# Kernel optimization log

Hardware: AMD Instinct MI355X
Metric: run time of the kernel (lower is better)

## Reference

```python
import jax, jax.numpy as jnp
import numpy as np

N = 50000
IN_F = 128
OUT_F = 128
NRELA = 128
E1 = 400000
E2 = 100000
ALPHA = 0.2   # LeakyReLU slope
D = 0.85      # PageRank damping
EPS = 1e-12


def setup_inputs() -> dict:
    key = jax.random.key(0)
    ks = jax.random.split(key, 8)
    return {
        "input": jax.random.normal(ks[0], (N, IN_F), dtype=jnp.float32),
        "edge": jax.random.randint(ks[1], (2, E1), 0, N, dtype=jnp.int64),
        "edge_embed": jax.random.normal(ks[2], (E1, NRELA), dtype=jnp.float32),
        "edge_list_nhop": jax.random.randint(ks[3], (2, E2), 0, N, dtype=jnp.int64),
        "edge_embed_nhop": jax.random.normal(ks[4], (E2, NRELA), dtype=jnp.float32),
        "entity_rank": jax.random.uniform(ks[5], (N,), dtype=jnp.float32),
        "a": 0.05 * jax.random.normal(ks[6], (OUT_F, 2 * IN_F + NRELA), dtype=jnp.float32),
        "a_2": 0.05 * jax.random.normal(ks[7], (1, OUT_F), dtype=jnp.float32),
    }


def reference(input, edge, edge_embed, edge_list_nhop, edge_embed_nhop, entity_rank, a, a_2):
    n = input.shape[0]
    # concat n-hop edges (len(edge_list_nhop) != 0 path in the original)
    e = jnp.concatenate([edge, edge_list_nhop], axis=1)          # [2, E]
    emb = jnp.concatenate([edge_embed, edge_embed_nhop], axis=0) # [E, nrela]
    src, dst = e[0], e[1]

    # edge MLP: edge_h = [x_src | x_dst | rel]  -> a @ edge_h^T, leakyrelu
    edge_h = jnp.concatenate([input[src], input[dst], emb], axis=1)   # [E, 2*in+nrela]
    edge_m = jax.nn.leaky_relu(edge_h @ a.T, ALPHA)                   # [E, out]
    powers = -jax.nn.leaky_relu(edge_m @ a_2[0], ALPHA)               # [E]
    edge_e = jnp.exp(powers)                                          # [E]

    # softmax-like normalization over incoming edges of each target node
    a_rowsum = jax.ops.segment_sum(edge_e, dst, num_segments=n)       # [N]
    a_rowsum = jnp.where(a_rowsum == 0.0, EPS, a_rowsum)
    rel_att = edge_e / a_rowsum[dst]                                  # [E]

    # PageRank-style rank update
    e_rowsum = jax.ops.segment_sum(rel_att, src, num_segments=n)      # [N] (out-sum)
    e_rowsum = jnp.where(e_rowsum == 0.0, EPS, e_rowsum)
    val = rel_att * entity_rank[src] / e_rowsum[src]                  # [E]
    e_colsum = jax.ops.segment_sum(val, dst, num_segments=n)          # [N]
    new_rank = 1.0 - D + D * e_colsum                                 # [N]

    # rank-weighted attention propagation of edge features
    edge_prop = (rel_att * new_rank[src])[:, None] * edge_m           # [E, out]
    h_prime = jax.ops.segment_sum(edge_prop, dst, num_segments=n)     # [N, out]

    return jax.nn.elu(h_prime), new_rank
```

## Files before the change

### kernel.cpp

```cpp
#include <hip/hip_runtime.h>
#include <math.h>

#define N_NODES 50000
#define E1N 400000
#define E2N 100000
#define E_TOT 500000
#define ALPHAC 0.2f
#define DAMP 0.85f
#define EPSC 1e-12f

typedef __bf16 bf16_t;
typedef __bf16 bf16x4 __attribute__((ext_vector_type(4)));
typedef __bf16 bf16x8 __attribute__((ext_vector_type(8)));
typedef float f32x16 __attribute__((ext_vector_type(16)));

__device__ __forceinline__ float lrelu(float x) { return x > 0.f ? x : ALPHAC * x; }

__global__ __launch_bounds__(256) void k_pack12(const float* __restrict__ a,
                                                bf16_t* __restrict__ bp) {
  int i = blockIdx.x * 256 + threadIdx.x;
  if (i >= 32768) return;
  int j = i & 7;
  int l = (i >> 3) & 63;
  int nt = (i >> 9) & 7;
  int ks = i >> 12;
  int c = nt * 32 + (l & 31);
  int o = (c < 128) ? c : c - 128;
  int koff = (c < 128) ? 0 : 128;
  int k = ks * 16 + ((l >> 5) << 3) + j;
  bp[i] = (bf16_t)a[o * 384 + koff + k];
}

__global__ __launch_bounds__(256) void k_pack3(const float* __restrict__ a,
                                               bf16_t* __restrict__ bp) {
  int i = blockIdx.x * 256 + threadIdx.x;
  if (i >= 16384) return;
  int j = i & 7;
  int l = (i >> 3) & 63;
  int nt = (i >> 9) & 3;
  int ks = i >> 11;
  int o = nt * 32 + (l & 31);
  int k = ks * 16 + ((l >> 5) << 3) + j;
  bp[i] = (bf16_t)a[o * 384 + 256 + k];
}

__global__ __launch_bounds__(256) void k_edges(const int* __restrict__ edge,
                                               const int* __restrict__ nhop,
                                               int* __restrict__ sidx,
                                               int* __restrict__ didx, int stride,
                                               int* __restrict__ cnt) {
  int e = blockIdx.x * 256 + threadIdx.x;
  if (e >= E_TOT) return;
  int s, d;
  if (e < E1N) {
    s = edge[(size_t)e * stride];
    d = edge[(size_t)(E1N + e) * stride];
  } else {
    int t = e - E1N;
    s = nhop[(size_t)t * stride];
    d = nhop[(size_t)(E2N + t) * stride];
  }
  sidx[e] = s;
  didx[e] = d;
  if (cnt) atomicAdd(&cnt[d], 1);
}

__global__ __launch_bounds__(256) void k_scan(const int* __restrict__ cnt,
                                              int* __restrict__ csr_start,
                                              int* __restrict__ cursor) {
  __shared__ int ls[256];
  __shared__ int lofs[256];
  int t = threadIdx.x;
  int lo = t * 196, hi = lo + 196;
  if (hi > N_NODES) hi = N_NODES;
  int s = 0;
  for (int i = lo; i < hi; ++i) s += cnt[i];
  ls[t] = s;
  __syncthreads();
  if (t == 0) {
    int run = 0;
    for (int i = 0; i < 256; ++i) { lofs[i] = run; run += ls[i]; }
  }
  __syncthreads();
  int run = lofs[t];
  for (int i = lo; i < hi; ++i) {
    csr_start[i] = run;
    cursor[i] = run;
    run += cnt[i];
  }
}

__global__ __launch_bounds__(256) void k_pos(const int* __restrict__ didx,
                                             int* __restrict__ cursor,
                                             int* __restrict__ eid) {
  int e = blockIdx.x * 256 + threadIdx.x;
  if (e >= E_TOT) return;
  int pos = atomicAdd(&cursor[didx[e]], 1);
  eid[pos] = e;
}

__global__ __launch_bounds__(256) void k_uv(const float* __restrict__ input,
                                            const bf16_t* __restrict__ bp12,
                                            bf16_t* __restrict__ uv) {
  const int tid = threadIdx.x, lane = tid & 63, wv = tid >> 6;
  const int n0 = blockIdx.x * 128 + wv * 32;
  const int m = lane & 31, hi2 = lane >> 5;
  int n = n0 + m;
  if (n >= N_NODES) n = 0;
  const float* ar = input + (size_t)n * 128 + hi2 * 8;
  const bf16x8* bp = (const bf16x8*)bp12;

  f32x16 acc[8];
#pragma unroll
  for (int nt = 0; nt < 8; ++nt)
#pragma unroll
    for (int r = 0; r < 16; ++r) acc[nt][r] = 0.f;

#pragma unroll
  for (int ks = 0; ks < 8; ++ks) {
    float4 u0 = *(const float4*)(ar + ks * 16);
    float4 u1 = *(const float4*)(ar + ks * 16 + 4);
    bf16x8 af = {(bf16_t)u0.x, (bf16_t)u0.y, (bf16_t)u0.z, (bf16_t)u0.w,
                 (bf16_t)u1.x, (bf16_t)u1.y, (bf16_t)u1.z, (bf16_t)u1.w};
#pragma unroll
    for (int nt = 0; nt < 8; ++nt)
      acc[nt] = __builtin_amdgcn_mfma_f32_32x32x16_bf16(af, bp[(ks * 8 + nt) * 64 + lane],
                                                        acc[nt], 0, 0, 0);
  }
#pragma unroll
  for (int nt = 0; nt < 8; ++nt)
#pragma unroll
    for (int r = 0; r < 16; ++r) {
      int row = (r & 3) + ((r >> 2) << 3) + (hi2 << 2);
      int node = n0 + row;
      if (node < N_NODES) uv[(size_t)node * 256 + nt * 32 + m] = (bf16_t)acc[nt][r];
    }
}

__global__ __launch_bounds__(256, 3) void k_passA(
    const float* __restrict__ eemb, const float* __restrict__ eembn,
    const bf16_t* __restrict__ uv, const int* __restrict__ sidx,
    const int* __restrict__ didx, const bf16_t* __restrict__ bp3,
    const float* __restrict__ a2, float* __restrict__ edge_e,
    float* __restrict__ a_rowsum, bf16_t* __restrict__ P) {
  __shared__ bf16_t s_sum[128][136];
  const int tid = threadIdx.x;
  const long long e0 = (long long)blockIdx.x * 128;

  {
    const int g = tid >> 5;
    const int cl = (tid & 31) * 4;
#pragma unroll
    for (int i = 0; i < 16; ++i) {
      int el = i * 8 + g;
      long long e = e0 + el;
      float sx = 0.f, sy = 0.f, sz = 0.f, sw = 0.f;
      if (e < E_TOT) {
        int s = sidx[e], d = didx[e];
        bf16x4 u = *(const bf16x4*)(uv + (size_t)s * 256 + cl);
        bf16x4 v = *(const bf16x4*)(uv + (size_t)d * 256 + 128 + cl);
        sx = (float)u[0] + (float)v[0];
        sy = (float)u[1] + (float)v[1];
        sz = (float)u[2] + (float)v[2];
        sw = (float)u[3] + (float)v[3];
      }
      bf16x4 o = {(bf16_t)sx, (bf16_t)sy, (bf16_t)sz, (bf16_t)sw};
      *(bf16x4*)&s_sum[el][cl] = o;
    }
  }
  __syncthreads();

  const int lane = tid & 63;
  const int wv = tid >> 6;
  const long long e0w = e0 + wv * 32;
  if (e0w >= E_TOT) return;
  const int m = lane & 31, hi2 = lane >> 5;
  const long long e = e0w + m;
  const float* b2 = (e < E1N) ? (eemb + (size_t)e * 128)
                              : (eembn + (size_t)(e - E1N) * 128);
  const float* ar = b2 + hi2 * 8;

  const bf16x8* bp = (const bf16x8*)bp3;
  f32x16 acc[4];
#pragma unroll
  for (int nt = 0; nt < 4; ++nt)
#pragma unroll
    for (int r = 0; r < 16; ++r) acc[nt][r] = 0.f;

  auto loadA = [&](int ks) -> bf16x8 {
    float4 u0 = *(const float4*)(ar + ks * 16);
    float4 u1 = *(const float4*)(ar + ks * 16 + 4);
    bf16x8 rr = {(bf16_t)u0.x, (bf16_t)u0.y, (bf16_t)u0.z, (bf16_t)u0.w,
                 (bf16_t)u1.x, (bf16_t)u1.y, (bf16_t)u1.z, (bf16_t)u1.w};
    return rr;
  };

  bf16x8 a_cur = loadA(0);
  bf16x8 bb[4], bn[4];
#pragma unroll
  for (int nt = 0; nt < 4; ++nt) bb[nt] = bp[nt * 64 + lane];

#pragma unroll
  for (int ks = 0; ks < 8; ++ks) {
    bf16x8 a_nxt;
    if (ks < 7) {
      a_nxt = loadA(ks + 1);
#pragma unroll
      for (int nt = 0; nt < 4; ++nt) bn[nt] = bp[((ks + 1) * 4 + nt) * 64 + lane];
    }
#pragma unroll
    for (int nt = 0; nt < 4; ++nt)
      acc[nt] = __builtin_amdgcn_mfma_f32_32x32x16_bf16(a_cur, bb[nt], acc[nt], 0, 0, 0);
    a_cur = a_nxt;
#pragma unroll
    for (int nt = 0; nt < 4; ++nt) bb[nt] = bn[nt];
  }

  bf16_t* Pt = P + ((long long)blockIdx.x * 4 + wv) * 4096;
  float sac[16];
#pragma unroll
  for (int r = 0; r < 16; ++r) sac[r] = 0.f;
#pragma unroll
  for (int nt = 0; nt < 4; ++nt) {
    int o = nt * 32 + m;
    float a2v = a2[o];
#pragma unroll
    for (int r = 0; r < 16; ++r) {
      int row = (r & 3) + ((r >> 2) << 3) + (hi2 << 2);
      float c = acc[nt][r] + (float)s_sum[wv * 32 + row][o];
      float p = lrelu(c);
      Pt[(nt * 16 + r) * 64 + lane] = (bf16_t)p;
      sac[r] += p * a2v;
    }
  }
#pragma unroll
  for (int off = 1; off < 32; off <<= 1) {
#pragma unroll
    for (int r = 0; r < 16; ++r) sac[r] += __shfl_xor(sac[r], off, 64);
  }
  if (m == 0) {
#pragma unroll
    for (int r = 0; r < 16; ++r) {
      int row = (r & 3) + ((r >> 2) << 3) + (hi2 << 2);
      long long ee_i = e0w + row;
      float ev = expf(-lrelu(sac[r]));
      edge_e[ee_i] = ev;
      atomicAdd(&a_rowsum[didx[ee_i]], ev);
    }
  }
}

__global__ __launch_bounds__(256) void k_hprime(const bf16_t* __restrict__ P,
                                                const int* __restrict__ eid,
                                                const int* __restrict__ csr_start,
                                                const int* __restrict__ cnt,
                                                const float* __restrict__ w,
                                                float* __restrict__ out) {
  int g = (blockIdx.x << 3) | (threadIdx.x >> 5);
  if (g >= N_NODES) return;
  int m = threadIdx.x & 31;
  int start = csr_start[g], deg = cnt[g];
  float a0 = 0.f, a1 = 0.f, a2v = 0.f, a3v = 0.f;
  for (int i = 0; i < deg; ++i) {
    int e = eid[start + i];
    float we = w[e];
    int row = e & 31;
    int r = (row & 3) | ((row >> 3) << 2);
    int hi2 = (row >> 2) & 1;
    const bf16_t* p = P + (long long)(e >> 5) * 4096 + r * 64 + hi2 * 32 + m;
    a0 += we * (float)p[0];
    a1 += we * (float)p[16 * 64];
    a2v += we * (float)p[32 * 64];
    a3v += we * (float)p[48 * 64];
  }
  float* o = out + (size_t)g * 128 + m;
  o[0] = a0 > 0.f ? a0 : expm1f(a0);
  o[32] = a1 > 0.f ? a1 : expm1f(a1);
  o[64] = a2v > 0.f ? a2v : expm1f(a2v);
  o[96] = a3v > 0.f ? a3v : expm1f(a3v);
}

template <bool ACCUM>
__global__ __launch_bounds__(256, 3) void k_pass(
    const float* __restrict__ eemb, const float* __restrict__ eembn,
    const bf16_t* __restrict__ uv, const int* __restrict__ sidx,
    const int* __restrict__ didx, const bf16_t* __restrict__ bp3,
    const float* __restrict__ a2, float* __restrict__ edge_e,
    float* __restrict__ a_rowsum, const float* __restrict__ rel_att,
    const float* __restrict__ new_rank, float* __restrict__ hout) {
  __shared__ bf16_t s_sum[128][136];
  const int tid = threadIdx.x;
  const long long e0 = (long long)blockIdx.x * 128;
  {
    const int g = tid >> 5;
    const int cl = (tid & 31) * 4;
#pragma unroll
    for (int i = 0; i < 16; ++i) {
      int el = i * 8 + g;
      long long e = e0 + el;
      float sx = 0.f, sy = 0.f, sz = 0.f, sw = 0.f;
      if (e < E_TOT) {
        int s = sidx[e], d = didx[e];
        bf16x4 u = *(const bf16x4*)(uv + (size_t)s * 256 + cl);
        bf16x4 v = *(const bf16x4*)(uv + (size_t)d * 256 + 128 + cl);
        sx = (float)u[0] + (float)v[0];
        sy = (float)u[1] + (float)v[1];
        sz = (float)u[2] + (float)v[2];
        sw = (float)u[3] + (float)v[3];
      }
      bf16x4 o = {(bf16_t)sx, (bf16_t)sy, (bf16_t)sz, (bf16_t)sw};
      *(bf16x4*)&s_sum[el][cl] = o;
    }
  }
  __syncthreads();

  const int lane = tid & 63;
  const int wv = tid >> 6;
  const long long e0w = e0 + wv * 32;
  if (e0w >= E_TOT) return;
  const int m = lane & 31, hi2 = lane >> 5;
  const long long e = e0w + m;
  const float* b2 = (e < E1N) ? (eemb + (size_t)e * 128)
                              : (eembn + (size_t)(e - E1N) * 128);
  const float* ar = b2 + hi2 * 8;

  const bf16x8* bp = (const bf16x8*)bp3;
  f32x16 acc[4];
#pragma unroll
  for (int nt = 0; nt < 4; ++nt)
#pragma unroll
    for (int r = 0; r < 16; ++r) acc[nt][r] = 0.f;

  auto loadA = [&](int ks) -> bf16x8 {
    float4 u0 = *(const float4*)(ar + ks * 16);
    float4 u1 = *(const float4*)(ar + ks * 16 + 4);
    bf16x8 rr = {(bf16_t)u0.x, (bf16_t)u0.y, (bf16_t)u0.z, (bf16_t)u0.w,
                 (bf16_t)u1.x, (bf16_t)u1.y, (bf16_t)u1.z, (bf16_t)u1.w};
    return rr;
  };

  bf16x8 a_cur = loadA(0);
  bf16x8 bb[4], bn[4];
#pragma unroll
  for (int nt = 0; nt < 4; ++nt) bb[nt] = bp[nt * 64 + lane];

#pragma unroll
  for (int ks = 0; ks < 8; ++ks) {
    bf16x8 a_nxt;
    if (ks < 7) {
      a_nxt = loadA(ks + 1);
#pragma unroll
      for (int nt = 0; nt < 4; ++nt) bn[nt] = bp[((ks + 1) * 4 + nt) * 64 + lane];
    }
#pragma unroll
    for (int nt = 0; nt < 4; ++nt)
      acc[nt] = __builtin_amdgcn_mfma_f32_32x32x16_bf16(a_cur, bb[nt], acc[nt], 0, 0, 0);
    a_cur = a_nxt;
#pragma unroll
    for (int nt = 0; nt < 4; ++nt) bb[nt] = bn[nt];
  }

  if (!ACCUM) {
    float sac[16];
#pragma unroll
    for (int r = 0; r < 16; ++r) sac[r] = 0.f;
#pragma unroll
    for (int nt = 0; nt < 4; ++nt) {
      float a2v = a2[nt * 32 + m];
      int o = nt * 32 + m;
#pragma unroll
      for (int r = 0; r < 16; ++r) {
        int row = (r & 3) + ((r >> 2) << 3) + (hi2 << 2);
        float c = acc[nt][r] + (float)s_sum[wv * 32 + row][o];
        sac[r] += lrelu(c) * a2v;
      }
    }
#pragma unroll
    for (int off = 1; off < 32; off <<= 1) {
#pragma unroll
      for (int r = 0; r < 16; ++r) sac[r] += __shfl_xor(sac[r], off, 64);
    }
    if (m == 0) {
#pragma unroll
      for (int r = 0; r < 16; ++r) {
        int row = (r & 3) + ((r >> 2) << 3) + (hi2 << 2);
        long long ee_i = e0w + row;
        float ev = expf(-lrelu(sac[r]));
        edge_e[ee_i] = ev;
        atomicAdd(&a_rowsum[didx[ee_i]], ev);
      }
    }
  } else {
    float w_m = rel_att[e] * new_rank[sidx[e]];
    int d = didx[e];
    float wr[16];
    int dr[16];
#pragma unroll
    for (int r = 0; r < 16; ++r) {
      int row = (r & 3) + ((r >> 2) << 3) + (hi2 << 2);
      wr[r] = __shfl(w_m, row, 64);
      dr[r] = __shfl(d, row, 64);
    }
#pragma unroll
    for (int nt = 0; nt < 4; ++nt) {
      int o = nt * 32 + m;
#pragma unroll
      for (int r = 0; r < 16; ++r) {
        int row = (r & 3) + ((r >> 2) << 3) + (hi2 << 2);
        float c = acc[nt][r] + (float)s_sum[wv * 32 + row][o];
        atomicAdd(&hout[(size_t)dr[r] * 128 + o], lrelu(c) * wr[r]);
      }
    }
  }
}

__global__ __launch_bounds__(256) void k_relatt(const float* __restrict__ edge_e,
                                                const int* __restrict__ didx,
                                                const int* __restrict__ sidx,
                                                const float* __restrict__ a_rowsum,
                                                float* __restrict__ rel_att,
                                                float* __restrict__ e_rowsum) {
  int e = blockIdx.x * 256 + threadIdx.x;
  if (e >= E_TOT) return;
  float rs = a_rowsum[didx[e]];
  rs = (rs == 0.f) ? EPSC : rs;
  float r = edge_e[e] / rs;
  rel_att[e] = r;
  atomicAdd(&e_rowsum[sidx[e]], r);
}

__global__ __launch_bounds__(256) void k_val(const float* __restrict__ rel_att,
                                             const int* __restrict__ sidx,
                                             const int* __restrict__ didx,
                                             const float* __restrict__ rank,
                                             const float* __restrict__ e_rowsum,
                                             float* __restrict__ e_colsum) {
  int e = blockIdx.x * 256 + threadIdx.x;
  if (e >= E_TOT) return;
  int s = sidx[e];
  float er = e_rowsum[s];
  er = (er == 0.f) ? EPSC : er;
  float val = rel_att[e] * rank[s] / er;
  atomicAdd(&e_colsum[didx[e]], val);
}

__global__ __launch_bounds__(256) void k_rank(const float* __restrict__ e_colsum,
                                              float* __restrict__ new_rank,
                                              float* __restrict__ out_tail) {
  int n = blockIdx.x * 256 + threadIdx.x;
  if (n >= N_NODES) return;
  float nr = 1.f - DAMP + DAMP * e_colsum[n];
  new_rank[n] = nr;
  out_tail[n] = nr;
}

__global__ __launch_bounds__(256) void k_w(const float* __restrict__ rel_att,
                                           const int* __restrict__ sidx,
                                           const float* __restrict__ new_rank,
                                           float* __restrict__ w) {
  int e = blockIdx.x * 256 + threadIdx.x;
  if (e < E_TOT) w[e] = rel_att[e] * new_rank[sidx[e]];
}

__global__ __launch_bounds__(256) void k_elu(float* __restrict__ h) {
  int i = blockIdx.x * 256 + threadIdx.x;
  if (i < N_NODES * 128) {
    float x = h[i];
    h[i] = x > 0.f ? x : expm1f(x);
  }
}

extern "C" void kernel_launch(void* const* d_in, const int* in_sizes, int n_in,
                              void* d_out, int out_size, void* d_ws, size_t ws_size,
                              hipStream_t stream) {
  const float* input = (const float*)d_in[0];
  const int* edge = (const int*)d_in[1];
  const float* eemb = (const float*)d_in[2];
  const int* enh = (const int*)d_in[3];
  const float* eembn = (const float*)d_in[4];
  const float* rank = (const float*)d_in[5];
  const float* a = (const float*)d_in[6];
  const float* a2 = (const float*)d_in[7];
  float* out = (float*)d_out;

  int estride = (in_sizes[1] == 2 * E1N) ? 1 : 2;

  char* ws = (char*)d_ws;
  bf16_t* bp12 = (bf16_t*)(ws);
  bf16_t* bp3 = (bf16_t*)(ws + 65536);
  bf16_t* uv = (bf16_t*)(ws + 98304);
  int* sidx = (int*)(ws + 25698304);
  int* didx = (int*)(ws + 27698304);
  float* edge_e = (float*)(ws + 29698304);
  float* rel_att = (float*)(ws + 31698304);
  float* warr = (float*)(ws + 33698304);
  int* eid = (int*)(ws + 35698304);
  int* csr_start = (int*)(ws + 37698304);
  int* cursor = (int*)(ws + 37898304);
  int* cnt = (int*)(ws + 38098304);
  float* a_rowsum = (float*)(ws + 38298304);
  float* e_rowsum = (float*)(ws + 38498304);
  float* e_colsum = (float*)(ws + 38698304);
  float* new_rank = (float*)(ws + 38898304);
  bf16_t* P = (bf16_t*)(ws + 39098304);

  const bool big = ws_size >= 167098304ULL;

  const int NB = (E_TOT + 127) / 128;
  const int EB = (E_TOT + 255) / 256;

  if (big) {
    hipMemsetAsync(cnt, 0, 4 * 200000, stream);

    k_pack12<<<128, 256, 0, stream>>>(a, bp12);
    k_pack3<<<64, 256, 0, stream>>>(a, bp3);
    k_edges<<<EB, 256, 0, stream>>>(edge, enh, sidx, didx, estride, cnt);
    k_scan<<<1, 256, 0, stream>>>(cnt, csr_start, cursor);
    k_pos<<<EB, 256, 0, stream>>>(didx, cursor, eid);
    k_uv<<<(N_NODES + 127) / 128, 256, 0, stream>>>(input, bp12, uv);

    k_passA<<<NB, 256, 0, stream>>>(eemb, eembn, uv, sidx, didx, bp3, a2,
                                    edge_e, a_rowsum, P);
    k_relatt<<<EB, 256, 0, stream>>>(edge_e, didx, sidx, a_rowsum, rel_att, e_rowsum);
    k_val<<<EB, 256, 0, stream>>>(rel_att, sidx, didx, rank, e_rowsum, e_colsum);
    k_rank<<<(N_NODES + 255) / 256, 256, 0, stream>>>(e_colsum, new_rank,
                                                      out + (size_t)N_NODES * 128);
    k_w<<<EB, 256, 0, stream>>>(rel_att, sidx, new_rank, warr);
    k_hprime<<<(N_NODES + 7) / 8, 256, 0, stream>>>(P, eid, csr_start, cnt, warr, out);
  } else {
    hipMemsetAsync(cnt, 0, 4 * 200000, stream);
    hipMemsetAsync(out, 0, (size_t)N_NODES * 128 * 4, stream);

    k_pack12<<<128, 256, 0, stream>>>(a, bp12);
    k_pack3<<<64, 256, 0, stream>>>(a, bp3);
    k_edges<<<EB, 256, 0, stream>>>(edge, enh, sidx, didx, estride, nullptr);
    k_uv<<<(N_NODES + 127) / 128, 256, 0, stream>>>(input, bp12, uv);

    k_pass<false><<<NB, 256, 0, stream>>>(eemb, eembn, uv, sidx, didx, bp3, a2,
                                          edge_e, a_rowsum, nullptr, nullptr, nullptr);
    k_relatt<<<EB, 256, 0, stream>>>(edge_e, didx, sidx, a_rowsum, rel_att, e_rowsum);
    k_val<<<EB, 256, 0, stream>>>(rel_att, sidx, didx, rank, e_rowsum, e_colsum);
    k_rank<<<(N_NODES + 255) / 256, 256, 0, stream>>>(e_colsum, new_rank,
                                                      out + (size_t)N_NODES * 128);
    k_pass<true><<<NB, 256, 0, stream>>>(eemb, eembn, uv, sidx, didx, bp3, a2,
                                         nullptr, nullptr, rel_att, new_rank, out);
    k_elu<<<(N_NODES * 128 + 255) / 256, 256, 0, stream>>>(out);
  }
}
```

Before: 744.0 us.

## Split edge pass into coalesced relation GEMM and per-edge gather kernel

The fused per-edge pass is replaced by two kernels. The first computes the relation-embedding GEMM with A staged through swizzled shared memory and stores row-major fp16 results. The second gathers the node projections, applies LeakyReLU, writes bf16 activations in place, and computes edge_e with one atomic per edge. P now uses a row-major per-edge layout, so h_prime reads vectorised bf16x4 rows and computes the weight inline instead of calling a separate k_w kernel. The split adds an extra round trip of the 500k x 128 intermediate through global memory in exchange for coalesced accesses.

```diff
diff --git a/kernel.cpp b/kernel.cpp
--- a/kernel.cpp
+++ b/kernel.cpp
@@ -12,6 +12,9 @@
 typedef __bf16 bf16_t;
 typedef __bf16 bf16x4 __attribute__((ext_vector_type(4)));
 typedef __bf16 bf16x8 __attribute__((ext_vector_type(8)));
+typedef _Float16 f16_t;
+typedef _Float16 f16x4 __attribute__((ext_vector_type(4)));
+typedef _Float16 f16x8 __attribute__((ext_vector_type(8)));
 typedef float f32x16 __attribute__((ext_vector_type(16)));
 
 __device__ __forceinline__ float lrelu(float x) { return x > 0.f ? x : ALPHAC * x; }
@@ -137,16 +140,162 @@
     }
 }
 
-__global__ __launch_bounds__(256, 3) void k_passA(
+__global__ __launch_bounds__(256, 4) void k_gemm3(const float* __restrict__ eemb,
+                                                  const float* __restrict__ eembn,
+                                                  const bf16_t* __restrict__ bp3,
+                                                  f16_t* __restrict__ w3) {
+  __shared__ __align__(16) char s_raw[32768];
+  const int tid = threadIdx.x;
+  const long long e0 = (long long)blockIdx.x * 128;
+
+  {
+    const int r8 = tid >> 5;
+    const int cb = (tid & 31) * 8;
+#pragma unroll
+    for (int i = 0; i < 16; ++i) {
+      int row = i * 8 + r8;
+      long long e = e0 + row;
+      float4 u = {0.f, 0.f, 0.f, 0.f};
+      if (e < E_TOT) {
+        const float* src = (e < E1N) ? eemb + (size_t)e * 128
+                                     : eembn + (size_t)(e - E1N) * 128;
+        u = *(const float4*)(src + (cb >> 1));
+      }
+      bf16x4 b = {(bf16_t)u.x, (bf16_t)u.y, (bf16_t)u.z, (bf16_t)u.w};
+      *(bf16x4*)(s_raw + row * 256 + (cb ^ ((row & 7) << 4))) = b;
+    }
+  }
+  __syncthreads();
+
+  const int lane = tid & 63, wv = tid >> 6;
+  const int m = lane & 31, hi2 = lane >> 5;
+  const int arow = wv * 32 + m;
+  const int swz = (arow & 7) << 4;
+  const bf16x8* bp = (const bf16x8*)bp3;
+
+  f32x16 acc[4];
+#pragma unroll
+  for (int nt = 0; nt < 4; ++nt)
+#pragma unroll
+    for (int r = 0; r < 16; ++r) acc[nt][r] = 0.f;
+
+  bf16x8 bb[4], bn[4];
+#pragma unroll
+  for (int nt = 0; nt < 4; ++nt) bb[nt] = bp[nt * 64 + lane];
+
+#pragma unroll
+  for (int ks = 0; ks < 8; ++ks) {
+    bf16x8 af = *(const bf16x8*)(s_raw + arow * 256 + ((ks * 32 + hi2 * 16) ^ swz));
+    if (ks < 7) {
+#pragma unroll
+      for (int nt = 0; nt < 4; ++nt) bn[nt] = bp[((ks + 1) * 4 + nt) * 64 + lane];
+    }
+#pragma unroll
+    for (int nt = 0; nt < 4; ++nt)
+      acc[nt] = __builtin_amdgcn_mfma_f32_32x32x16_bf16(af, bb[nt], acc[nt], 0, 0, 0);
+#pragma unroll
+    for (int nt = 0; nt < 4; ++nt) bb[nt] = bn[nt];
+  }
+  __syncthreads();
+
+#pragma unroll
+  for (int nt = 0; nt < 4; ++nt)
+#pragma unroll
+    for (int r = 0; r < 16; ++r) {
+      int orow = (r & 3) + ((r >> 2) << 3) + (hi2 << 2);
+      int row = wv * 32 + orow;
+      int cb = (nt * 32 + m) * 2;
+      *(f16_t*)(s_raw + row * 256 + (cb ^ ((row & 7) << 4))) = (f16_t)acc[nt][r];
+    }
+  __syncthreads();
+
+  {
+    const int rr = tid >> 4;
+    const int cb = (tid & 15) * 16;
+#pragma unroll
+    for (int i = 0; i < 8; ++i) {
+      int row = i * 16 + rr;
+      long long e = e0 + row;
+      if (e < E_TOT) {
+        f16x8 v = *(const f16x8*)(s_raw + row * 256 + (cb ^ ((row & 7) << 4)));
+        *(f16x8*)(w3 + (size_t)e * 128 + (cb >> 1)) = v;
+      }
+    }
+  }
+}
+
+__global__ __launch_bounds__(256) void k_passB(const bf16_t* __restrict__ uv,
+                                               const int* __restrict__ sidx,
+                                               const int* __restrict__ didx,
+                                               f16_t* __restrict__ w3,
+                                               const float* __restrict__ a2,
+                                               float* __restrict__ edge_e,
+                                               float* __restrict__ a_rowsum) {
+  long long e = (long long)blockIdx.x * 8 + (threadIdx.x >> 5);
+  if (e >= E_TOT) return;
+  const int m = threadIdx.x & 31;
+  int s = sidx[e], d = didx[e];
+  bf16x4 u = *(const bf16x4*)(uv + (size_t)s * 256 + m * 4);
+  bf16x4 v = *(const bf16x4*)(uv + (size_t)d * 256 + 128 + m * 4);
+  f16x4 w = *(const f16x4*)(w3 + (size_t)e * 128 + m * 4);
+  float4 a2v = *(const float4*)(a2 + m * 4);
+  float p0 = lrelu((float)u[0] + (float)v[0] + (float)w[0]);
+  float p1 = lrelu((float)u[1] + (float)v[1] + (float)w[1]);
+  float p2 = lrelu((float)u[2] + (float)v[2] + (float)w[2]);
+  float p3 = lrelu((float)u[3] + (float)v[3] + (float)w[3]);
+  bf16x4 po = {(bf16_t)p0, (bf16_t)p1, (bf16_t)p2, (bf16_t)p3};
+  *(f16x4*)(w3 + (size_t)e * 128 + m * 4) = __builtin_bit_cast(f16x4, po);
+  float sac = p0 * a2v.x + p1 * a2v.y + p2 * a2v.z + p3 * a2v.w;
+#pragma unroll
+  for (int off = 1; off < 32; off <<= 1) sac += __shfl_xor(sac, off, 64);
+  if (m == 0) {
+    float ev = expf(-lrelu(sac));
+    edge_e[e] = ev;
+    atomicAdd(&a_rowsum[d], ev);
+  }
+}
+
+__global__ __launch_bounds__(256) void k_hprime(const bf16_t* __restrict__ P,
+                                                const int* __restrict__ eid,
+                                                const int* __restrict__ csr_start,
+                                                const int* __restrict__ cnt,
+                                                const float* __restrict__ rel_att,
+                                                const int* __restrict__ sidx,
+                                                const float* __restrict__ new_rank,
+                                                float* __restrict__ out) {
+  int g = (blockIdx.x << 3) | (threadIdx.x >> 5);
+  if (g >= N_NODES) return;
+  int m = threadIdx.x & 31;
+  int start = csr_start[g], deg = cnt[g];
+  float a0 = 0.f, a1 = 0.f, a2v = 0.f, a3v = 0.f;
+  for (int i = 0; i < deg; ++i) {
+    int e = eid[start + i];
+    float we = rel_att[e] * new_rank[sidx[e]];
+    bf16x4 p = *(const bf16x4*)(P + (size_t)e * 128 + m * 4);
+    a0 += we * (float)p[0];
+    a1 += we * (float)p[1];
+    a2v += we * (float)p[2];
+    a3v += we * (float)p[3];
+  }
+  float4 r;
+  r.x = a0 > 0.f ? a0 : expm1f(a0);
+  r.y = a1 > 0.f ? a1 : expm1f(a1);
+  r.z = a2v > 0.f ? a2v : expm1f(a2v);
+  r.w = a3v > 0.f ? a3v : expm1f(a3v);
+  *(float4*)(out + (size_t)g * 128 + m * 4) = r;
+}
+
+template <bool ACCUM>
+__global__ __launch_bounds__(256, 3) void k_pass(
     const float* __restrict__ eemb, const float* __restrict__ eembn,
     const bf16_t* __restrict__ uv, const int* __restrict__ sidx,
     const int* __restrict__ didx, const bf16_t* __restrict__ bp3,
     const float* __restrict__ a2, float* __restrict__ edge_e,
-    float* __restrict__ a_rowsum, bf16_t* __restrict__ P) {
+    float* __restrict__ a_rowsum, const float* __restrict__ rel_att,
+    const float* __restrict__ new_rank, float* __restrict__ hout) {
   __shared__ bf16_t s_sum[128][136];
   const int tid = threadIdx.x;
   const long long e0 = (long long)blockIdx.x * 128;
-
   {
     const int g = tid >> 5;
     const int cl = (tid & 31) * 4;
@@ -216,150 +365,6 @@
     for (int nt = 0; nt < 4; ++nt) bb[nt] = bn[nt];
   }
 
-  bf16_t* Pt = P + ((long long)blockIdx.x * 4 + wv) * 4096;
-  float sac[16];
-#pragma unroll
-  for (int r = 0; r < 16; ++r) sac[r] = 0.f;
-#pragma unroll
-  for (int nt = 0; nt < 4; ++nt) {
-    int o = nt * 32 + m;
-    float a2v = a2[o];
-#pragma unroll
-    for (int r = 0; r < 16; ++r) {
-      int row = (r & 3) + ((r >> 2) << 3) + (hi2 << 2);
-      float c = acc[nt][r] + (float)s_sum[wv * 32 + row][o];
-      float p = lrelu(c);
-      Pt[(nt * 16 + r) * 64 + lane] = (bf16_t)p;
-      sac[r] += p * a2v;
-    }
-  }
-#pragma unroll
-  for (int off = 1; off < 32; off <<= 1) {
-#pragma unroll
-    for (int r = 0; r < 16; ++r) sac[r] += __shfl_xor(sac[r], off, 64);
-  }
-  if (m == 0) {
-#pragma unroll
-    for (int r = 0; r < 16; ++r) {
-      int row = (r & 3) + ((r >> 2) << 3) + (hi2 << 2);
-      long long ee_i = e0w + row;
-      float ev = expf(-lrelu(sac[r]));
-      edge_e[ee_i] = ev;
-      atomicAdd(&a_rowsum[didx[ee_i]], ev);
-    }
-  }
-}
-
-__global__ __launch_bounds__(256) void k_hprime(const bf16_t* __restrict__ P,
-                                                const int* __restrict__ eid,
-                                                const int* __restrict__ csr_start,
-                                                const int* __restrict__ cnt,
-                                                const float* __restrict__ w,
-                                                float* __restrict__ out) {
-  int g = (blockIdx.x << 3) | (threadIdx.x >> 5);
-  if (g >= N_NODES) return;
-  int m = threadIdx.x & 31;
-  int start = csr_start[g], deg = cnt[g];
-  float a0 = 0.f, a1 = 0.f, a2v = 0.f, a3v = 0.f;
-  for (int i = 0; i < deg; ++i) {
-    int e = eid[start + i];
-    float we = w[e];
-    int row = e & 31;
-    int r = (row & 3) | ((row >> 3) << 2);
-    int hi2 = (row >> 2) & 1;
-    const bf16_t* p = P + (long long)(e >> 5) * 4096 + r * 64 + hi2 * 32 + m;
-    a0 += we * (float)p[0];
-    a1 += we * (float)p[16 * 64];
-    a2v += we * (float)p[32 * 64];
-    a3v += we * (float)p[48 * 64];
-  }
-  float* o = out + (size_t)g * 128 + m;
-  o[0] = a0 > 0.f ? a0 : expm1f(a0);
-  o[32] = a1 > 0.f ? a1 : expm1f(a1);
-  o[64] = a2v > 0.f ? a2v : expm1f(a2v);
-  o[96] = a3v > 0.f ? a3v : expm1f(a3v);
-}
-
-template <bool ACCUM>
-__global__ __launch_bounds__(256, 3) void k_pass(
-    const float* __restrict__ eemb, const float* __restrict__ eembn,
-    const bf16_t* __restrict__ uv, const int* __restrict__ sidx,
-    const int* __restrict__ didx, const bf16_t* __restrict__ bp3,
-    const float* __restrict__ a2, float* __restrict__ edge_e,
-    float* __restrict__ a_rowsum, const float* __restrict__ rel_att,
-    const float* __restrict__ new_rank, float* __restrict__ hout) {
-  __shared__ bf16_t s_sum[128][136];
-  const int tid = threadIdx.x;
-  const long long e0 = (long long)blockIdx.x * 128;
-  {
-    const int g = tid >> 5;
-    const int cl = (tid & 31) * 4;
-#pragma unroll
-    for (int i = 0; i < 16; ++i) {
-      int el = i * 8 + g;
-      long long e = e0 + el;
-      float sx = 0.f, sy = 0.f, sz = 0.f, sw = 0.f;
-      if (e < E_TOT) {
-        int s = sidx[e], d = didx[e];
-        bf16x4 u = *(const bf16x4*)(uv + (size_t)s * 256 + cl);
-        bf16x4 v = *(const bf16x4*)(uv + (size_t)d * 256 + 128 + cl);
-        sx = (float)u[0] + (float)v[0];
-        sy = (float)u[1] + (float)v[1];
-        sz = (float)u[2] + (float)v[2];
-        sw = (float)u[3] + (float)v[3];
-      }
-      bf16x4 o = {(bf16_t)sx, (bf16_t)sy, (bf16_t)sz, (bf16_t)sw};
-      *(bf16x4*)&s_sum[el][cl] = o;
-    }
-  }
-  __syncthreads();
-
-  const int lane = tid & 63;
-  const int wv = tid >> 6;
-  const long long e0w = e0 + wv * 32;
-  if (e0w >= E_TOT) return;
-  const int m = lane & 31, hi2 = lane >> 5;
-  const long long e = e0w + m;
-  const float* b2 = (e < E1N) ? (eemb + (size_t)e * 128)
-                              : (eembn + (size_t)(e - E1N) * 128);
-  const float* ar = b2 + hi2 * 8;
-
-  const bf16x8* bp = (const bf16x8*)bp3;
-  f32x16 acc[4];
-#pragma unroll
-  for (int nt = 0; nt < 4; ++nt)
-#pragma unroll
-    for (int r = 0; r < 16; ++r) acc[nt][r] = 0.f;
-
-  auto loadA = [&](int ks) -> bf16x8 {
-    float4 u0 = *(const float4*)(ar + ks * 16);
-    float4 u1 = *(const float4*)(ar + ks * 16 + 4);
-    bf16x8 rr = {(bf16_t)u0.x, (bf16_t)u0.y, (bf16_t)u0.z, (bf16_t)u0.w,
-                 (bf16_t)u1.x, (bf16_t)u1.y, (bf16_t)u1.z, (bf16_t)u1.w};
-    return rr;
-  };
-
-  bf16x8 a_cur = loadA(0);
-  bf16x8 bb[4], bn[4];
-#pragma unroll
-  for (int nt = 0; nt < 4; ++nt) bb[nt] = bp[nt * 64 + lane];
-
-#pragma unroll
-  for (int ks = 0; ks < 8; ++ks) {
-    bf16x8 a_nxt;
-    if (ks < 7) {
-      a_nxt = loadA(ks + 1);
-#pragma unroll
-      for (int nt = 0; nt < 4; ++nt) bn[nt] = bp[((ks + 1) * 4 + nt) * 64 + lane];
-    }
-#pragma unroll
-    for (int nt = 0; nt < 4; ++nt)
-      acc[nt] = __builtin_amdgcn_mfma_f32_32x32x16_bf16(a_cur, bb[nt], acc[nt], 0, 0, 0);
-    a_cur = a_nxt;
-#pragma unroll
-    for (int nt = 0; nt < 4; ++nt) bb[nt] = bn[nt];
-  }
-
   if (!ACCUM) {
     float sac[16];
 #pragma unroll
@@ -454,14 +459,6 @@
   out_tail[n] = nr;
 }
 
-__global__ __launch_bounds__(256) void k_w(const float* __restrict__ rel_att,
-                                           const int* __restrict__ sidx,
-                                           const float* __restrict__ new_rank,
-                                           float* __restrict__ w) {
-  int e = blockIdx.x * 256 + threadIdx.x;
-  if (e < E_TOT) w[e] = rel_att[e] * new_rank[sidx[e]];
-}
-
 __global__ __launch_bounds__(256) void k_elu(float* __restrict__ h) {
   int i = blockIdx.x * 256 + threadIdx.x;
   if (i < N_NODES * 128) {
@@ -493,7 +490,6 @@
   int* didx = (int*)(ws + 27698304);
   float* edge_e = (float*)(ws + 29698304);
   float* rel_att = (float*)(ws + 31698304);
-  float* warr = (float*)(ws + 33698304);
   int* eid = (int*)(ws + 35698304);
   int* csr_start = (int*)(ws + 37698304);
   int* cursor = (int*)(ws + 37898304);
@@ -519,14 +515,15 @@
     k_pos<<<EB, 256, 0, stream>>>(didx, cursor, eid);
     k_uv<<<(N_NODES + 127) / 128, 256, 0, stream>>>(input, bp12, uv);
 
-    k_passA<<<NB, 256, 0, stream>>>(eemb, eembn, uv, sidx, didx, bp3, a2,
-                                    edge_e, a_rowsum, P);
+    k_gemm3<<<NB, 256, 0, stream>>>(eemb, eembn, bp3, (f16_t*)P);
+    k_passB<<<(E_TOT + 7) / 8, 256, 0, stream>>>(uv, sidx, didx, (f16_t*)P, a2,
+                                                 edge_e, a_rowsum);
     k_relatt<<<EB, 256, 0, stream>>>(edge_e, didx, sidx, a_rowsum, rel_att, e_rowsum);
     k_val<<<EB, 256, 0, stream>>>(rel_att, sidx, didx, rank, e_rowsum, e_colsum);
     k_rank<<<(N_NODES + 255) / 256, 256, 0, stream>>>(e_colsum, new_rank,
                                                       out + (size_t)N_NODES * 128);
-    k_w<<<EB, 256, 0, stream>>>(rel_att, sidx, new_rank, warr);
-    k_hprime<<<(N_NODES + 7) / 8, 256, 0, stream>>>(P, eid, csr_start, cnt, warr, out);
+    k_hprime<<<(N_NODES + 7) / 8, 256, 0, stream>>>(P, eid, csr_start, cnt, rel_att,
+                                                    sidx, new_rank, out);
   } else {
     hipMemsetAsync(cnt, 0, 4 * 200000, stream);
     hipMemsetAsync(out, 0, (size_t)N_NODES * 128 * 4, stream);
```

Measured after the change: 776.0 us. +4.3%, slower.
